# Kernel optimization log

Measured on AMD Instinct MI355X. Metric: run time of the kernel, lower is better.

Reference implementation:

```python
import jax, jax.numpy as jnp
import numpy as np

N, P, T, K = 20000, 5, 16, 3
IN, H, O = 150, 64, 128


def setup_inputs() -> dict:
    key = jax.random.key(0)
    k1, k2, k3, k4, k5 = jax.random.split(key, 5)
    x = jax.random.normal(k1, (N, IN), dtype=jnp.float32)
    conn_idx = jax.random.randint(k2, (N, P, T, K), 0, N, dtype=jnp.int32)
    conn_w = jax.random.uniform(k3, (N, P, T, K), dtype=jnp.float32)
    # learned params
    W1 = jax.random.normal(k4, (H, IN), dtype=jnp.float32) * 0.05   # linear_1 (no bias)
    Wg = jax.random.normal(k5, (O, H, P, T), dtype=jnp.float32) * 0.05  # geodesic conv weight
    bg = jnp.zeros((O,), dtype=jnp.float32)                          # geodesic conv bias
    return {"x": x, "conn_idx": conn_idx, "conn_w": conn_w, "W1": W1, "Wg": Wg, "bg": bg}


def reference(x, conn_idx, conn_w, W1, Wg, bg):
    # Linear + ReLU: [N, H]
    h = jax.nn.relu(x @ W1.T)
    # Geodesic patch gather: interpolate vertex features into P x T bins
    g = jnp.take(h, conn_idx, axis=0)                 # [N, P, T, K, H]
    patches = jnp.einsum('nptk,nptkh->npth', conn_w, g)  # [N, P, T, H]
    # Geodesic convolution: contract patch bins and channels
    out = jnp.einsum('npth,ohpt->no', patches, Wg) + bg  # [N, O]
    # L2 normalize per vertex
    norm = jnp.linalg.norm(out, axis=-1, keepdims=True)
    return out / norm
```

## Files before the change

### kernel.cpp

```cpp
#include <hip/hip_runtime.h>
#include <hip/hip_fp16.h>

#define NV   20000
#define KK   3
#define INF  150
#define HH   64
#define OO   128
#define PT   80
#define KTOT 5120
#define NB   32
#define BS2  72
#define RS2  152
#define CHB  (NB * RS2)
#define XS   168
#define NSUB 10

typedef _Float16 fh8 __attribute__((ext_vector_type(8)));
typedef __attribute__((ext_vector_type(4))) float f32x4;

__device__ __forceinline__ unsigned short f2h(float f) {
    return __half_as_ushort(__float2half(f));
}
__device__ __forceinline__ float h2f(unsigned short u) {
    return __half2float(__ushort_as_half(u));
}

struct Conn { int idx[6]; float w[6]; };

__global__ __launch_bounds__(256) void prep_kernel(
    const float* __restrict__ Wg, const float* __restrict__ x,
    const float* __restrict__ W1, unsigned short* __restrict__ W2,
    unsigned short* __restrict__ hb) {
    __shared__ __align__(16) unsigned char smem[32256];
    const int tid = threadIdx.x;

    if (blockIdx.x < 128) {
        float* lds = (float*)smem;
        const int o = blockIdx.x;
        const float* src = Wg + o * KTOT;
        for (int t = tid; t < KTOT; t += 256) {
            int h = t / 80, bin = t - h * 80;
            lds[h * 81 + bin] = src[t];
        }
        __syncthreads();
        for (int t = tid; t < KTOT; t += 256) {
            W2[(t >> 5) * 4096 + o * 32 + (t & 31)] =
                f2h(lds[(t & 63) * 81 + (t >> 6)]);
        }
        return;
    }

    unsigned short* xs = (unsigned short*)smem;
    unsigned short* ws = xs + 32 * XS;
    const int n0 = (blockIdx.x - 128) * 32;

    for (int e = tid; e < 32 * INF; e += 256) {
        int r = e / INF, c = e - r * INF;
        xs[r * XS + c] = f2h(x[n0 * INF + e]);
    }
    for (int e = tid; e < 32 * 18; e += 256) {
        int r = e / 18, c = e - r * 18;
        xs[r * XS + 150 + c] = 0;
    }
    for (int e = tid; e < 64 * INF; e += 256) {
        int r = e / INF, c = e - r * INF;
        ws[r * XS + c] = f2h(W1[e]);
    }
    for (int e = tid; e < 64 * 18; e += 256) {
        int r = e / 18, c = e - r * 18;
        ws[r * XS + 150 + c] = 0;
    }
    __syncthreads();

    const int wv   = tid >> 6;
    const int lane = tid & 63;
    const int q    = lane >> 4;
    const int r16  = lane & 15;
    const int o0   = wv * 16;

    f32x4 acc0 = {0.f, 0.f, 0.f, 0.f};
    f32x4 acc1 = acc0;
    #pragma unroll
    for (int s = 0; s < 5; s++) {
        const int kb = s * 32 + q * 8;
        fh8 a0 = *(const fh8*)(xs + r16 * XS + kb);
        fh8 a1 = *(const fh8*)(xs + (16 + r16) * XS + kb);
        fh8 b  = *(const fh8*)(ws + (o0 + r16) * XS + kb);
        acc0 = __builtin_amdgcn_mfma_f32_16x16x32_f16(a0, b, acc0, 0, 0, 0);
        acc1 = __builtin_amdgcn_mfma_f32_16x16x32_f16(a1, b, acc1, 0, 0, 0);
    }
    #pragma unroll
    for (int r = 0; r < 4; r++) {
        float v0 = acc0[r] > 0.f ? acc0[r] : 0.f;
        float v1 = acc1[r] > 0.f ? acc1[r] : 0.f;
        hb[(n0 + q * 4 + r) * HH + o0 + r16]      = f2h(v0);
        hb[(n0 + 16 + q * 4 + r) * HH + o0 + r16] = f2h(v1);
    }
}

__global__ __launch_bounds__(256, 4) void geo_kernel(
    const int*   __restrict__ conn_idx, const float* __restrict__ conn_w,
    const unsigned short* __restrict__ W2, const unsigned short* __restrict__ hb,
    float* __restrict__ out, unsigned short* __restrict__ parts) {
    __shared__ __align__(16) unsigned short pch[2 * CHB];
    __shared__ int   ci[NB * 60];
    __shared__ float cw[NB * 60];

    const int tid  = threadIdx.x;
    const int ks   = blockIdx.x & 3;
    const int n0   = (blockIdx.x >> 2) * NB;
    const int wv   = tid >> 6;
    const int lane = tid & 63;
    const int q    = lane >> 4;
    const int r16  = lane & 15;
    const int j8   = tid & 7;
    const int bl   = (tid >> 3) & 1;
    const int ng   = tid >> 4;
    const int bbase = ks * 20;
    const int Sbase = ks * 40;

    for (int e = tid; e < NB * 60; e += 256) {
        const int r = e / 60, c = e - r * 60;
        const int g = (n0 + r) * (PT * KK) + bbase * KK + c;
        ci[e] = conn_idx[g];
        cw[e] = conn_w[g];
    }

    f32x4 acc00 = {0.f, 0.f, 0.f, 0.f};
    f32x4 acc01 = acc00, acc10 = acc00, acc11 = acc00;

    Conn cN;
    fh8  hv[6];

    auto loadc = [&](int cc, Conn& c) {
        const int bo = (cc * 2 + bl) * 3;
        #pragma unroll
        for (int i = 0; i < 2; i++) {
            const int base = (ng + i * 16) * 60 + bo;
            c.idx[i * 3 + 0] = ci[base];
            c.idx[i * 3 + 1] = ci[base + 1];
            c.idx[i * 3 + 2] = ci[base + 2];
            c.w[i * 3 + 0]   = cw[base];
            c.w[i * 3 + 1]   = cw[base + 1];
            c.w[i * 3 + 2]   = cw[base + 2];
        }
    };
    auto loadh = [&](const Conn& c) {
        #pragma unroll
        for (int t = 0; t < 6; t++)
            hv[t] = *(const fh8*)(hb + c.idx[t] * HH + j8 * 8);
    };
    auto cwrite = [&](const Conn& c, unsigned short* buf) {
        #pragma unroll
        for (int i = 0; i < 2; i++) {
            const int n = ng + i * 16;
            _Float16 w0 = (_Float16)c.w[i * 3 + 0];
            _Float16 w1 = (_Float16)c.w[i * 3 + 1];
            _Float16 w2 = (_Float16)c.w[i * 3 + 2];
            fh8 W0 = {w0, w0, w0, w0, w0, w0, w0, w0};
            fh8 W1v = {w1, w1, w1, w1, w1, w1, w1, w1};
            fh8 W2v = {w2, w2, w2, w2, w2, w2, w2, w2};
            fh8 r = hv[i * 3] * W0 + hv[i * 3 + 1] * W1v + hv[i * 3 + 2] * W2v;
            *(fh8*)(buf + n * RS2 + bl * BS2 + j8 * 8) = r;
        }
    };
    auto mfmaph = [&](const unsigned short* buf, int cc) {
        #pragma unroll
        for (int s = 0; s < 4; s++) {
            const int S  = Sbase + cc * 4 + s;
            const int ao = (s >> 1) * BS2 + (s & 1) * 32 + q * 8;
            fh8 a0 = *(const fh8*)(buf + r16 * RS2 + ao);
            fh8 a1 = *(const fh8*)(buf + (16 + r16) * RS2 + ao);
            fh8 b0 = *(const fh8*)(W2 + S * 4096 + (wv * 32 + r16) * 32 + q * 8);
            fh8 b1 = *(const fh8*)(W2 + S * 4096 + (wv * 32 + 16 + r16) * 32 + q * 8);
            acc00 = __builtin_amdgcn_mfma_f32_16x16x32_f16(a0, b0, acc00, 0, 0, 0);
            acc01 = __builtin_amdgcn_mfma_f32_16x16x32_f16(a0, b1, acc01, 0, 0, 0);
            acc10 = __builtin_amdgcn_mfma_f32_16x16x32_f16(a1, b0, acc10, 0, 0, 0);
            acc11 = __builtin_amdgcn_mfma_f32_16x16x32_f16(a1, b1, acc11, 0, 0, 0);
        }
    };

    __syncthreads();

    loadc(0, cN);
    loadh(cN);
    cwrite(cN, pch);
    __syncthreads();

    for (int cc = 0; cc < NSUB; cc++) {
        if (cc + 1 < NSUB) {
            loadc(cc + 1, cN);
            loadh(cN);
        }
        mfmaph(&pch[(cc & 1) * CHB], cc);
        if (cc + 1 < NSUB) cwrite(cN, &pch[((cc + 1) & 1) * CHB]);
        __syncthreads();
    }

    const int o0 = wv * 32;
    if (ks == 0) {
        #pragma unroll
        for (int r = 0; r < 4; r++) {
            out[(n0 + q * 4 + r) * OO + o0 + r16]           = acc00[r];
            out[(n0 + q * 4 + r) * OO + o0 + 16 + r16]      = acc01[r];
            out[(n0 + 16 + q * 4 + r) * OO + o0 + r16]      = acc10[r];
            out[(n0 + 16 + q * 4 + r) * OO + o0 + 16 + r16] = acc11[r];
        }
    } else {
        unsigned short* pp = parts + (ks - 1) * (NV * OO);
        #pragma unroll
        for (int r = 0; r < 4; r++) {
            pp[(n0 + q * 4 + r) * OO + o0 + r16]           = f2h(acc00[r]);
            pp[(n0 + q * 4 + r) * OO + o0 + 16 + r16]      = f2h(acc01[r]);
            pp[(n0 + 16 + q * 4 + r) * OO + o0 + r16]      = f2h(acc10[r]);
            pp[(n0 + 16 + q * 4 + r) * OO + o0 + 16 + r16] = f2h(acc11[r]);
        }
    }
}

__global__ __launch_bounds__(256) void norm_kernel(
    float* __restrict__ out, const unsigned short* __restrict__ parts,
    const float* __restrict__ bg) {
    const int tid = threadIdx.x;
    const int n   = blockIdx.x * 32 + (tid >> 3);
    const int l   = tid & 7;
    float v[16];
    float s = 0.f;
    #pragma unroll
    for (int i = 0; i < 16; i++) {
        const int o = i * 8 + l;
        const int e = n * OO + o;
        v[i] = out[e] + h2f(parts[e]) + h2f(parts[NV * OO + e]) +
               h2f(parts[2 * NV * OO + e]) + bg[o];
        s += v[i] * v[i];
    }
    for (int off = 4; off; off >>= 1) s += __shfl_down(s, off, 8);
    const float r = rsqrtf(__shfl(s, 0, 8));
    #pragma unroll
    for (int i = 0; i < 16; i++)
        out[n * OO + i * 8 + l] = v[i] * r;
}

extern "C" void kernel_launch(void* const* d_in, const int* in_sizes, int n_in,
                              void* d_out, int out_size, void* d_ws, size_t ws_size,
                              hipStream_t stream) {
    const float* x        = (const float*)d_in[0];
    const int*   conn_idx = (const int*)  d_in[1];
    const float* conn_w   = (const float*)d_in[2];
    const float* W1       = (const float*)d_in[3];
    const float* Wg       = (const float*)d_in[4];
    const float* bg       = (const float*)d_in[5];
    float*       out      = (float*)d_out;

    unsigned short* W2    = (unsigned short*)d_ws;
    unsigned short* hb    = W2 + OO * KTOT;
    unsigned short* parts = hb + NV * HH;

    hipLaunchKernelGGL(prep_kernel, dim3(128 + NV / 32), dim3(256), 0, stream,
                       Wg, x, W1, W2, hb);
    hipLaunchKernelGGL(geo_kernel, dim3(4 * NV / NB), dim3(256), 0, stream,
                       conn_idx, conn_w, W2, hb, out, parts);
    hipLaunchKernelGGL(norm_kernel, dim3(NV / 32), dim3(256), 0, stream,
                       out, parts, bg);
}
```

Baseline: 181.8 us.

## Widen geo kernel tile to 64 vertices with 512 threads and compact connectivity

The geodesic conv kernel now handles 64 vertices per block using 512 threads (8 waves split into 2 row-halves by 4 output-column pairs), which halves how often each W2 slice is reloaded per vertex. The pipeline now steps one bin at a time (20 steps) instead of two bins per step. Connection indices and weights are stored in LDS as 16-bit values to cut shared memory use, and the grid is rounded up with bounds checks on the tail. The costs are more barriers per block and a reliance on vertex indices fitting in 16 bits.

```diff
diff --git a/kernel.cpp b/kernel.cpp
--- a/kernel.cpp
+++ b/kernel.cpp
@@ -8,12 +8,11 @@
 #define OO   128
 #define PT   80
 #define KTOT 5120
-#define NB   32
-#define BS2  72
-#define RS2  152
-#define CHB  (NB * RS2)
+#define NB   64
+#define RS   72
+#define CB   (NB * RS)
 #define XS   168
-#define NSUB 10
+#define NBIN 20
 
 typedef _Float16 fh8 __attribute__((ext_vector_type(8)));
 typedef __attribute__((ext_vector_type(4))) float f32x4;
@@ -24,8 +23,9 @@
 __device__ __forceinline__ float h2f(unsigned short u) {
     return __half2float(__ushort_as_half(u));
 }
-
-struct Conn { int idx[6]; float w[6]; };
+__device__ __forceinline__ _Float16 u2h(unsigned short u) {
+    union { unsigned short s; _Float16 h; } c; c.s = u; return c.h;
+}
 
 __global__ __launch_bounds__(256) void prep_kernel(
     const float* __restrict__ Wg, const float* __restrict__ x,
@@ -98,13 +98,13 @@
     }
 }
 
-__global__ __launch_bounds__(256, 4) void geo_kernel(
+__global__ __launch_bounds__(512, 6) void geo_kernel(
     const int*   __restrict__ conn_idx, const float* __restrict__ conn_w,
     const unsigned short* __restrict__ W2, const unsigned short* __restrict__ hb,
     float* __restrict__ out, unsigned short* __restrict__ parts) {
-    __shared__ __align__(16) unsigned short pch[2 * CHB];
-    __shared__ int   ci[NB * 60];
-    __shared__ float cw[NB * 60];
+    __shared__ __align__(16) unsigned short pch[2 * CB];
+    __shared__ unsigned short ci[NB * 60];
+    __shared__ unsigned short cw[NB * 60];
 
     const int tid  = threadIdx.x;
     const int ks   = blockIdx.x & 3;
@@ -113,66 +113,57 @@
     const int lane = tid & 63;
     const int q    = lane >> 4;
     const int r16  = lane & 15;
+    const int mp   = wv & 1;
+    const int op   = wv >> 1;
     const int j8   = tid & 7;
-    const int bl   = (tid >> 3) & 1;
-    const int ng   = tid >> 4;
-    const int bbase = ks * 20;
+    const int vg   = tid >> 3;
+    const int bbase = ks * NBIN;
     const int Sbase = ks * 40;
 
-    for (int e = tid; e < NB * 60; e += 256) {
+    for (int e = tid; e < NB * 60; e += 512) {
         const int r = e / 60, c = e - r * 60;
-        const int g = (n0 + r) * (PT * KK) + bbase * KK + c;
-        ci[e] = conn_idx[g];
-        cw[e] = conn_w[g];
+        const int v = n0 + r;
+        if (v < NV) {
+            const int g = v * (PT * KK) + bbase * KK + c;
+            ci[e] = (unsigned short)conn_idx[g];
+            cw[e] = f2h(conn_w[g]);
+        } else {
+            ci[e] = 0;
+            cw[e] = 0;
+        }
     }
 
     f32x4 acc00 = {0.f, 0.f, 0.f, 0.f};
     f32x4 acc01 = acc00, acc10 = acc00, acc11 = acc00;
 
-    Conn cN;
-    fh8  hv[6];
-
-    auto loadc = [&](int cc, Conn& c) {
-        const int bo = (cc * 2 + bl) * 3;
-        #pragma unroll
-        for (int i = 0; i < 2; i++) {
-            const int base = (ng + i * 16) * 60 + bo;
-            c.idx[i * 3 + 0] = ci[base];
-            c.idx[i * 3 + 1] = ci[base + 1];
-            c.idx[i * 3 + 2] = ci[base + 2];
-            c.w[i * 3 + 0]   = cw[base];
-            c.w[i * 3 + 1]   = cw[base + 1];
-            c.w[i * 3 + 2]   = cw[base + 2];
-        }
+    fh8 hv0, hv1, hv2;
+    unsigned short w0u, w1u, w2u;
+
+    auto loadg = [&](int cc) {
+        const int base = vg * 60 + cc * 3;
+        const int i0 = ci[base], i1 = ci[base + 1], i2 = ci[base + 2];
+        w0u = cw[base]; w1u = cw[base + 1]; w2u = cw[base + 2];
+        hv0 = *(const fh8*)(hb + i0 * HH + j8 * 8);
+        hv1 = *(const fh8*)(hb + i1 * HH + j8 * 8);
+        hv2 = *(const fh8*)(hb + i2 * HH + j8 * 8);
     };
-    auto loadh = [&](const Conn& c) {
-        #pragma unroll
-        for (int t = 0; t < 6; t++)
-            hv[t] = *(const fh8*)(hb + c.idx[t] * HH + j8 * 8);
-    };
-    auto cwrite = [&](const Conn& c, unsigned short* buf) {
-        #pragma unroll
-        for (int i = 0; i < 2; i++) {
-            const int n = ng + i * 16;
-            _Float16 w0 = (_Float16)c.w[i * 3 + 0];
-            _Float16 w1 = (_Float16)c.w[i * 3 + 1];
-            _Float16 w2 = (_Float16)c.w[i * 3 + 2];
-            fh8 W0 = {w0, w0, w0, w0, w0, w0, w0, w0};
-            fh8 W1v = {w1, w1, w1, w1, w1, w1, w1, w1};
-            fh8 W2v = {w2, w2, w2, w2, w2, w2, w2, w2};
-            fh8 r = hv[i * 3] * W0 + hv[i * 3 + 1] * W1v + hv[i * 3 + 2] * W2v;
-            *(fh8*)(buf + n * RS2 + bl * BS2 + j8 * 8) = r;
-        }
+    auto cwr = [&](unsigned short* buf) {
+        const _Float16 w0 = u2h(w0u), w1 = u2h(w1u), w2 = u2h(w2u);
+        const fh8 W0 = {w0, w0, w0, w0, w0, w0, w0, w0};
+        const fh8 W1v = {w1, w1, w1, w1, w1, w1, w1, w1};
+        const fh8 W2v = {w2, w2, w2, w2, w2, w2, w2, w2};
+        fh8 r = hv0 * W0 + hv1 * W1v + hv2 * W2v;
+        *(fh8*)(buf + vg * RS + j8 * 8) = r;
     };
     auto mfmaph = [&](const unsigned short* buf, int cc) {
         #pragma unroll
-        for (int s = 0; s < 4; s++) {
-            const int S  = Sbase + cc * 4 + s;
-            const int ao = (s >> 1) * BS2 + (s & 1) * 32 + q * 8;
-            fh8 a0 = *(const fh8*)(buf + r16 * RS2 + ao);
-            fh8 a1 = *(const fh8*)(buf + (16 + r16) * RS2 + ao);
-            fh8 b0 = *(const fh8*)(W2 + S * 4096 + (wv * 32 + r16) * 32 + q * 8);
-            fh8 b1 = *(const fh8*)(W2 + S * 4096 + (wv * 32 + 16 + r16) * 32 + q * 8);
+        for (int s = 0; s < 2; s++) {
+            const int S  = Sbase + cc * 2 + s;
+            const int ao = s * 32 + q * 8;
+            fh8 a0 = *(const fh8*)(buf + (mp * 32 + r16) * RS + ao);
+            fh8 a1 = *(const fh8*)(buf + (mp * 32 + 16 + r16) * RS + ao);
+            fh8 b0 = *(const fh8*)(W2 + S * 4096 + ((op * 2 + 0) * 16 + r16) * 32 + q * 8);
+            fh8 b1 = *(const fh8*)(W2 + S * 4096 + ((op * 2 + 1) * 16 + r16) * 32 + q * 8);
             acc00 = __builtin_amdgcn_mfma_f32_16x16x32_f16(a0, b0, acc00, 0, 0, 0);
             acc01 = __builtin_amdgcn_mfma_f32_16x16x32_f16(a0, b1, acc01, 0, 0, 0);
             acc10 = __builtin_amdgcn_mfma_f32_16x16x32_f16(a1, b0, acc10, 0, 0, 0);
@@ -182,38 +173,41 @@
 
     __syncthreads();
 
-    loadc(0, cN);
-    loadh(cN);
-    cwrite(cN, pch);
+    loadg(0);
+    cwr(pch);
     __syncthreads();
 
-    for (int cc = 0; cc < NSUB; cc++) {
-        if (cc + 1 < NSUB) {
-            loadc(cc + 1, cN);
-            loadh(cN);
-        }
-        mfmaph(&pch[(cc & 1) * CHB], cc);
-        if (cc + 1 < NSUB) cwrite(cN, &pch[((cc + 1) & 1) * CHB]);
+    for (int cc = 0; cc < NBIN; cc++) {
+        if (cc + 1 < NBIN) loadg(cc + 1);
+        mfmaph(&pch[(cc & 1) * CB], cc);
+        if (cc + 1 < NBIN) cwr(&pch[((cc + 1) & 1) * CB]);
         __syncthreads();
     }
 
-    const int o0 = wv * 32;
     if (ks == 0) {
         #pragma unroll
-        for (int r = 0; r < 4; r++) {
-            out[(n0 + q * 4 + r) * OO + o0 + r16]           = acc00[r];
-            out[(n0 + q * 4 + r) * OO + o0 + 16 + r16]      = acc01[r];
-            out[(n0 + 16 + q * 4 + r) * OO + o0 + r16]      = acc10[r];
-            out[(n0 + 16 + q * 4 + r) * OO + o0 + 16 + r16] = acc11[r];
+        for (int a = 0; a < 2; a++) {
+            const int rb = n0 + (2 * mp + a) * 16 + q * 4;
+            #pragma unroll
+            for (int r = 0; r < 4; r++) {
+                if (rb + r < NV) {
+                    out[(rb + r) * OO + (2 * op + 0) * 16 + r16] = a ? acc10[r] : acc00[r];
+                    out[(rb + r) * OO + (2 * op + 1) * 16 + r16] = a ? acc11[r] : acc01[r];
+                }
+            }
         }
     } else {
         unsigned short* pp = parts + (ks - 1) * (NV * OO);
         #pragma unroll
-        for (int r = 0; r < 4; r++) {
-            pp[(n0 + q * 4 + r) * OO + o0 + r16]           = f2h(acc00[r]);
-            pp[(n0 + q * 4 + r) * OO + o0 + 16 + r16]      = f2h(acc01[r]);
-            pp[(n0 + 16 + q * 4 + r) * OO + o0 + r16]      = f2h(acc10[r]);
-            pp[(n0 + 16 + q * 4 + r) * OO + o0 + 16 + r16] = f2h(acc11[r]);
+        for (int a = 0; a < 2; a++) {
+            const int rb = n0 + (2 * mp + a) * 16 + q * 4;
+            #pragma unroll
+            for (int r = 0; r < 4; r++) {
+                if (rb + r < NV) {
+                    pp[(rb + r) * OO + (2 * op + 0) * 16 + r16] = f2h(a ? acc10[r] : acc00[r]);
+                    pp[(rb + r) * OO + (2 * op + 1) * 16 + r16] = f2h(a ? acc11[r] : acc01[r]);
+                }
+            }
         }
     }
 }
@@ -258,7 +252,7 @@
 
     hipLaunchKernelGGL(prep_kernel, dim3(128 + NV / 32), dim3(256), 0, stream,
                        Wg, x, W1, W2, hb);
-    hipLaunchKernelGGL(geo_kernel, dim3(4 * NV / NB), dim3(256), 0, stream,
+    hipLaunchKernelGGL(geo_kernel, dim3(4 * 313), dim3(512), 0, stream,
                        conn_idx, conn_w, W2, hb, out, parts);
     hipLaunchKernelGGL(norm_kernel, dim3(NV / 32), dim3(256), 0, stream,
                        out, parts, bg);
```

Result: no change. 180.5 us (-0.7%).
